# Performance work log

Hardware: AMD Instinct MI355X
Metric: run time of the kernel (lower is better)

Reference implementation:

```python
import jax, jax.numpy as jnp
import numpy as np
import math

B, T, C, H, LC, DFF = 2, 1024, 1024, 16, 256, 4096
EPS = 1e-6


def _ln(x):
    # LayerNorm without affine (elementwise_affine=False under AdaLN), eps=1e-6
    m = jnp.mean(x, -1, keepdims=True)
    v = jnp.mean((x - m) ** 2, -1, keepdims=True)
    return (x - m) * jax.lax.rsqrt(v + EPS)


def _heads(t):
    b, l, c = t.shape
    return t.reshape(b, l, H, c // H).transpose(0, 2, 1, 3)  # (b,H,l,dh)


def _unheads(t):
    b, h, l, d = t.shape
    return t.transpose(0, 2, 1, 3).reshape(b, l, h * d)


def setup_inputs():
    key = jax.random.key(0)
    ks = jax.random.split(key, 16)
    s = 0.02
    p = lambda k, sh: jax.random.normal(k, sh, jnp.float32) * s
    x_star = jax.random.normal(ks[0], (B, T, C), jnp.float32)
    x_hat = jax.random.normal(ks[1], (B, T, C), jnp.float32)
    c = jax.random.normal(ks[2], (B, LC, C), jnp.float32)
    chunk = jnp.sort(jax.random.randint(ks[3], (B, T), 0, 32), axis=1)
    m_star = chunk[:, :, None] > chunk[:, None, :]   # attend to strictly earlier chunks
    m_hat = chunk[:, :, None] == chunk[:, None, :]   # attend within same chunk
    dep_mask = jax.random.bernoulli(ks[4], 0.98, (B, T, T)) | jnp.eye(T, dtype=bool)[None]
    return dict(
        x_star=x_star, x_hat=x_hat, c=c,
        m_star=m_star, m_hat=m_hat, dep_mask=dep_mask,
        ncond_g=jnp.ones((C,), jnp.float32), ncond_b=jnp.zeros((C,), jnp.float32),
        Wq=p(ks[5], (C, C)), bq=jnp.zeros((C,), jnp.float32),
        Wkv=p(ks[6], (C, 2 * C)), bkv=jnp.zeros((2 * C,), jnp.float32),
        Wco=p(ks[7], (C, C)), bco=jnp.zeros((C,), jnp.float32),
        Wada=p(ks[8], (C, 6 * C)), bada=jnp.zeros((6 * C,), jnp.float32),
        Wqkv=p(ks[9], (C, 3 * C)), bqkv=jnp.zeros((3 * C,), jnp.float32),
        Wo=p(ks[10], (C, C)), bo=jnp.zeros((C,), jnp.float32),
        W1=p(ks[11], (C, DFF)), b1=jnp.zeros((DFF,), jnp.float32),
        W2=p(ks[12], (DFF, C)), b2=jnp.zeros((C,), jnp.float32),
    )


def _cross_attn(x, c, Wq, bq, Wkv, bkv, Wco, bco):
    q = _heads(x @ Wq + bq)
    k, v = jnp.split(c @ Wkv + bkv, 2, -1)
    k, v = _heads(k), _heads(v)
    att = jnp.einsum('bhtd,bhsd->bhts', q, k) / math.sqrt(C // H)
    y = jnp.einsum('bhts,bhsd->bhtd', jax.nn.softmax(att, -1), v)
    return _unheads(y) @ Wco + bco


def _interleave(xs, xh, m_star, m_hat, dep, Wqkv, bqkv, Wo, bo):
    # Attention.forward_interleave (eval: dropout identity)
    NEG = -jnp.inf
    sc = 1.0 / math.sqrt(C // H)
    qkv = lambda x: [_heads(t) for t in jnp.split(x @ Wqkv + bqkv, 3, -1)]
    qs, ks, vs = qkv(xs)
    qh, kh, vh = qkv(xh)
    blk_star = (~m_star)[:, None]     # True -> block
    blk_hat = (~m_hat)[:, None]
    blk_dep = (~dep)[:, None]
    causal = jnp.triu(jnp.ones((T, T), bool), 1)[None, None]
    # star stream: causal + dependency mask
    att_star = jnp.einsum('bhtd,bhsd->bhts', qs, ks) * sc
    att_star = jnp.where(blk_dep, NEG, att_star)
    p_star = jax.nn.softmax(jnp.where(causal, NEG, att_star), -1)
    y_star = _unheads(jnp.einsum('bhts,bhsd->bhtd', p_star, vs)) @ Wo + bo
    # hat stream: merge logits (q_hat vs k_star on earlier chunks, q_hat vs k_hat within chunk)
    a1 = jnp.where(blk_star, NEG, jnp.einsum('bhtd,bhsd->bhts', qh, ks) * sc)
    a2 = jnp.where(blk_hat, NEG, jnp.einsum('bhtd,bhsd->bhts', qh, kh) * sc)
    merged = jnp.where(jnp.isinf(a2), a1, a2)
    merged = jnp.where(blk_dep, NEG, merged)
    p_hat = jax.nn.softmax(merged, -1)
    y_hat = jnp.einsum('bhts,bhsd->bhtd', jnp.where(blk_star, 0.0, p_hat), vs) \
          + jnp.einsum('bhts,bhsd->bhtd', jnp.where(blk_hat, 0.0, p_hat), vh)
    y_hat = _unheads(y_hat) @ Wo + bo
    return y_star, y_hat


def reference(x_star, x_hat, c, m_star, m_hat, dep_mask,
              ncond_g, ncond_b, Wq, bq, Wkv, bkv, Wco, bco, Wada, bada,
              Wqkv, bqkv, Wo, bo, W1, b1, W2, b2):
    mod = lambda x, sh, scale: x * (1 + scale) + sh
    mlp = lambda x: jax.nn.gelu(x @ W1 + b1, approximate=True) @ W2 + b2
    ca = lambda x: _cross_attn(_ln(x) * ncond_g + ncond_b, c, Wq, bq, Wkv, bkv, Wco, bco)
    ada = lambda t: jnp.split(jax.nn.silu(t) @ Wada + bada, 6, -1)
    gs = ada(ca(x_star))
    gh = ada(ca(x_hat))
    ms = mod(_ln(x_star), gs[0], gs[1])
    mh = mod(_ln(x_hat), gh[0], gh[1])
    ys, yh = _interleave(ms, mh, m_star, m_hat, dep_mask, Wqkv, bqkv, Wo, bo)
    x_star = x_star + gs[2] * ys
    x_hat = x_hat + gh[2] * yh
    x_star = x_star + gs[5] * mlp(mod(_ln(x_star), gs[3], gs[4]))
    x_hat = x_hat + gh[5] * mlp(mod(_ln(x_hat), gh[3], gh[4]))
    return x_star, x_hat
```

## Files before the change

kernel.cpp:

```cpp
#include <hip/hip_runtime.h>
#include <hip/hip_bf16.h>
#include <stdint.h>

#define DEVI __device__ __forceinline__

typedef __bf16 bf16x8 __attribute__((ext_vector_type(8)));
typedef float f32x4 __attribute__((ext_vector_type(4)));
typedef unsigned short us;
typedef unsigned long long ull;

DEVI float b2f(us u) { union { unsigned int i; float f; } v; v.i = ((unsigned int)u) << 16; return v.f; }
DEVI us f2b(float f) {
  union { unsigned int i; float f; } v; v.f = f;
  unsigned int r = (v.i + 0x7fffu + ((v.i >> 16) & 1u)) >> 16;
  return (us)r;
}

#define NEGINF (-__builtin_inff())

DEVI void gl2lds16(const us* g, us* l) {
  __builtin_amdgcn_global_load_lds(
      (const __attribute__((address_space(1))) unsigned int*)g,
      (__attribute__((address_space(3))) unsigned int*)l, 16, 0, 0);
}

__global__ __launch_bounds__(256) void detect_flags(
    const unsigned int* __restrict__ xw, const unsigned int* __restrict__ mw,
    int* __restrict__ flags) {
  const int t = threadIdx.x;
  int cnt = 0, big = 0;
  for (int i = t; i < 4096; i += 256) {
    unsigned int w = xw[i];
    us lo = (us)(w & 0xffffu);
    float a = fabsf(b2f(lo));
    cnt += ((lo == 0) || (a >= 1e-8f && a <= 256.f)) ? 1 : 0;
    big |= (mw[i] > 1u) ? 1 : 0;
  }
  for (int o = 32; o; o >>= 1) { cnt += __shfl_down(cnt, o); big |= __shfl_down(big, o); }
  __shared__ int sc[4], sb[4];
  if ((t & 63) == 0) { sc[t >> 6] = cnt; sb[t >> 6] = big; }
  __syncthreads();
  if (t == 0) {
    flags[0] = (sc[0] + sc[1] + sc[2] + sc[3] < 2048) ? 1 : 0;
    flags[1] = (sb[0] | sb[1] | sb[2] | sb[3]);
  }
}

__global__ __launch_bounds__(256) void cvt_bf16(
    const void* __restrict__ src, us* __restrict__ dst, int n,
    const int* __restrict__ flags) {
  const int f32mode = flags[0];
  int idx = (blockIdx.x * 256 + threadIdx.x) * 4;
  if (idx >= n) return;
  if (f32mode) {
    const float* s = (const float*)src;
    float4 v = *(const float4*)(s + idx);
    dst[idx] = f2b(v.x); dst[idx + 1] = f2b(v.y);
    dst[idx + 2] = f2b(v.z); dst[idx + 3] = f2b(v.w);
  } else {
    *(uint2*)(dst + idx) = *(const uint2*)((const us*)src + idx);
  }
}

struct P10 { const void* p[10]; };
__global__ __launch_bounds__(256) void cvt_small(P10 ps, us* __restrict__ dst,
                                                 const int* __restrict__ flags) {
  const int offs[11] = {0, 1024, 2048, 3072, 5120, 6144, 12288, 15360, 16384, 20480, 21504};
  int idx = blockIdx.x * 256 + threadIdx.x;
  if (idx >= 21504) return;
  int seg = 0;
#pragma unroll
  for (int i = 1; i < 10; ++i) seg += (idx >= offs[i]) ? 1 : 0;
  int local = idx - offs[seg];
  float v = flags[0] ? ((const float*)ps.p[seg])[local]
                     : b2f(((const us*)ps.p[seg])[local]);
  dst[idx] = f2b(v);
}

__global__ __launch_bounds__(256) void transpose_cvt64(
    const void* __restrict__ W, us* __restrict__ WT, int K, int N,
    const int* __restrict__ flags) {
  __shared__ __attribute__((aligned(16))) us tile[64 * 72];
  const int f32m = flags[0];
  const int k0 = blockIdx.x * 64, n0 = blockIdx.y * 64;
  const int t = threadIdx.x;
  const int row = t >> 2, colb = (t & 3) * 16;
  const int sw = ((row >> 4) & 3) << 4;
  us tmp[16];
  if (f32m) {
    const float* src = (const float*)W + (size_t)(k0 + row) * N + n0 + colb;
#pragma unroll
    for (int i = 0; i < 16; i += 4) {
      float4 v = *(const float4*)(src + i);
      tmp[i] = f2b(v.x); tmp[i + 1] = f2b(v.y); tmp[i + 2] = f2b(v.z); tmp[i + 3] = f2b(v.w);
    }
  } else {
    const us* src = (const us*)W + (size_t)(k0 + row) * N + n0 + colb;
    *(uint4*)tmp = *(const uint4*)src;
    *(uint4*)(tmp + 8) = *(const uint4*)(src + 8);
  }
  *(uint4*)&tile[row * 72 + (colb ^ sw)] = *(uint4*)tmp;
  *(uint4*)&tile[row * 72 + (colb ^ sw) + 8] = *(uint4*)(tmp + 8);
  __syncthreads();
  const int orow = t >> 2, ocolb = (t & 3) * 16;
  const int pc = (orow & 15) | ((orow & 48) ^ (ocolb & 48));
  us out[16];
#pragma unroll
  for (int i = 0; i < 16; ++i) out[i] = tile[(ocolb + i) * 72 + pc];
  us* dst = WT + (size_t)(n0 + orow) * K + k0 + ocolb;
  *(uint4*)dst = *(uint4*)out;
  *(uint4*)(dst + 8) = *(uint4*)(out + 8);
}

struct P3 { const void* p[3]; };
__global__ __launch_bounds__(256) void pack_mask3(P3 ms, ull* __restrict__ bits,
                                                  const int* __restrict__ flags) {
  const int bytemode = flags[1];
  const void* m = ms.p[blockIdx.y];
  ull* out = bits + (size_t)blockIdx.y * 32768;
  int wv = blockIdx.x * 4 + (threadIdx.x >> 6);
  int lane = threadIdx.x & 63;
  for (int w = 0; w < 16; ++w) {
    int v;
    if (bytemode) v = ((const unsigned char*)m)[(size_t)wv * 1024 + w * 64 + lane];
    else          v = ((const int*)m)[(size_t)wv * 1024 + w * 64 + lane];
    ull b = __ballot(v != 0);
    if (lane == 0) out[(size_t)wv * 16 + w] = b;
  }
}

__global__ __launch_bounds__(256) void hat_blockflags(
    const ull* __restrict__ starb, const ull* __restrict__ hatb, int* __restrict__ bf) {
  const int bt = blockIdx.x;
  const int b = bt >> 4, tt = bt & 15;
  const int t = threadIdx.x, wv = t >> 6, lane = t & 63;
  const int t0 = tt * 64;
  for (int k = 0; k < 4; ++k) {
    int ck = wv * 4 + k;
    ull sw = starb[(size_t)(b * 1024 + t0 + lane) * 16 + ck];
    ull hw = hatb[(size_t)(b * 1024 + t0 + lane) * 16 + ck];
    int f = (__ballot(sw != 0ull) ? 1 : 0) | (__ballot(hw != 0ull) ? 2 : 0);
    if (lane == 0) bf[bt * 16 + ck] = f;
  }
}

__global__ __launch_bounds__(256) void vtrans(
    const us* __restrict__ src, us* __restrict__ dst,
    int T, int stride, int colBase, int rowOff) {
  __shared__ __attribute__((aligned(16))) us tile[64][65];
  const int bh = blockIdx.y, b = bh >> 4, h = bh & 15;
  const int t0 = blockIdx.x * 64;
  const int t = threadIdx.x;
#pragma unroll
  for (int it = 0; it < 2; ++it) {
    int idx = it * 256 + t; int r = idx >> 3, c8 = (idx & 7) * 8;
    uint4 d4 = *(const uint4*)(src + (size_t)(rowOff + b * T + t0 + r) * stride + colBase + h * 64 + c8);
    const us* e = (const us*)&d4;
#pragma unroll
    for (int i = 0; i < 8; ++i) tile[r][c8 + i] = e[i];
  }
  __syncthreads();
#pragma unroll
  for (int it = 0; it < 2; ++it) {
    int idx = it * 256 + t; int d = idx >> 3, c8 = (idx & 7) * 8;
    us tmp[8];
#pragma unroll
    for (int i = 0; i < 8; ++i) tmp[i] = tile[c8 + i][d];
    *(uint4*)(dst + ((size_t)(bh * 64 + d)) * T + t0 + c8) = *(const uint4*)tmp;
  }
}

__global__ __launch_bounds__(256) void ln_affine(
    const void* __restrict__ xs, const void* __restrict__ xh,
    const us* __restrict__ gw, const us* __restrict__ bw,
    us* __restrict__ lnx, us* __restrict__ xn, const int* __restrict__ flags) {
  const int f32m = flags[0];
  const int row = blockIdx.x;
  const void* xp = (row < 2048) ? xs : xh;
  const size_t base = (size_t)(row & 2047) * 1024;
  const int t = threadIdx.x;
  float v[4]; float s = 0.f, ss = 0.f;
#pragma unroll
  for (int i = 0; i < 4; ++i) {
    size_t idx = base + i * 256 + t;
    float x = f32m ? ((const float*)xp)[idx] : b2f(((const us*)xp)[idx]);
    v[i] = x; s += x; ss += x * x;
  }
  for (int o = 32; o; o >>= 1) { s += __shfl_down(s, o); ss += __shfl_down(ss, o); }
  __shared__ float red[2][4];
  const int wv = t >> 6, lane = t & 63;
  if (lane == 0) { red[0][wv] = s; red[1][wv] = ss; }
  __syncthreads();
  s = red[0][0] + red[0][1] + red[0][2] + red[0][3];
  ss = red[1][0] + red[1][1] + red[1][2] + red[1][3];
  const float mean = s * (1.f / 1024.f);
  const float var = fmaxf(ss * (1.f / 1024.f) - mean * mean, 0.f);
  const float rstd = rsqrtf(var + 1e-6f);
  const size_t ro = (size_t)row * 1024;
#pragma unroll
  for (int i = 0; i < 4; ++i) {
    int c = i * 256 + t;
    float n = (v[i] - mean) * rstd;
    lnx[ro + c] = f2b(n);
    xn[ro + c] = f2b(n * b2f(gw[c]) + b2f(bw[c]));
  }
}

__global__ __launch_bounds__(256) void mod_ms(
    const us* __restrict__ lnx, const us* __restrict__ gada, us* __restrict__ ms) {
  const size_t idx = ((size_t)blockIdx.x * 256 + threadIdx.x) * 4;
  const int row = (int)(idx >> 10), c = (int)(idx & 1023);
  const size_t gb = (size_t)row * 6144;
#pragma unroll
  for (int i = 0; i < 4; ++i) {
    float sh = b2f(gada[gb + c + i]);
    float sc = b2f(gada[gb + 1024 + c + i]);
    ms[idx + i] = f2b(b2f(lnx[idx + i]) * (1.f + sc) + sh);
  }
}

__global__ __launch_bounds__(256) void ln_mod(
    const float* __restrict__ x1, const us* __restrict__ gada, us* __restrict__ m2) {
  const int row = blockIdx.x;
  const float* xp = x1 + (size_t)row * 1024;
  const int t = threadIdx.x;
  float v[4]; float s = 0.f, ss = 0.f;
#pragma unroll
  for (int i = 0; i < 4; ++i) { float x = xp[i * 256 + t]; v[i] = x; s += x; ss += x * x; }
  for (int o = 32; o; o >>= 1) { s += __shfl_down(s, o); ss += __shfl_down(ss, o); }
  __shared__ float red[2][4];
  const int wv = t >> 6, lane = t & 63;
  if (lane == 0) { red[0][wv] = s; red[1][wv] = ss; }
  __syncthreads();
  s = red[0][0] + red[0][1] + red[0][2] + red[0][3];
  ss = red[1][0] + red[1][1] + red[1][2] + red[1][3];
  const float mean = s * (1.f / 1024.f);
  const float var = fmaxf(ss * (1.f / 1024.f) - mean * mean, 0.f);
  const float rstd = rsqrtf(var + 1e-6f);
  const size_t gb = (size_t)row * 6144;
#pragma unroll
  for (int i = 0; i < 4; ++i) {
    int c = i * 256 + t;
    float n = (v[i] - mean) * rstd;
    float sh = b2f(gada[gb + 3072 + c]);
    float sc = b2f(gada[gb + 4096 + c]);
    m2[(size_t)row * 1024 + c] = f2b(n * (1.f + sc) + sh);
  }
}

enum { EPI_BF16 = 0, EPI_SILU, EPI_GELU, EPI_GATE_XRES, EPI_GATE_OUT };

template <int EPI>
DEVI void gemm_epi(float v, int gmr, int gn, int N, void* out,
                   const us* gate, const void* res0, const void* res1,
                   const int* oflags) {
  const size_t oi = (size_t)gmr * N + gn;
  if constexpr (EPI == EPI_BF16) {
    ((us*)out)[oi] = f2b(v);
  } else if constexpr (EPI == EPI_SILU) {
    ((us*)out)[oi] = f2b(v / (1.f + __expf(-v)));
  } else if constexpr (EPI == EPI_GELU) {
    float u = 0.7978845608028654f * (v + 0.044715f * v * v * v);
    float th = 1.f - 2.f / (__expf(2.f * u) + 1.f);
    ((us*)out)[oi] = f2b(0.5f * v * (1.f + th));
  } else if constexpr (EPI == EPI_GATE_XRES) {
    float g = b2f(gate[(size_t)gmr * 6144 + gn]);
    const void* xr = (gmr < 2048) ? res0 : res1;
    size_t xi = (size_t)(gmr & 2047) * 1024 + gn;
    float x = oflags[0] ? ((const float*)xr)[xi] : b2f(((const us*)xr)[xi]);
    ((float*)out)[oi] = x + g * v;
  } else {
    float g = b2f(gate[(size_t)gmr * 6144 + gn]);
    float x = ((const float*)res0)[oi];
    float r2 = x + g * v;
    if (oflags[0]) ((float*)out)[oi] = r2;
    else ((us*)out)[oi] = f2b(r2);
  }
}

template <int EPI>
__global__ __launch_bounds__(256) void gemm_bt(
    const us* __restrict__ A, const us* __restrict__ BT,
    const us* __restrict__ bias, void* __restrict__ out,
    int M, int N, int K,
    const us* __restrict__ gate,
    const void* __restrict__ res0, const void* __restrict__ res1,
    const int* __restrict__ oflags) {
  __shared__ __attribute__((aligned(16))) us As[2][128 * 32];
  __shared__ __attribute__((aligned(16))) us Bs[2][128 * 32];
  const int m0 = blockIdx.x * 128, n0 = blockIdx.y * 128;
  const int t = threadIdx.x;
  const int wave = t >> 6, lane = t & 63;
  const int wm = (wave >> 1) * 64, wn = (wave & 1) * 64;
  const int l16 = lane & 15, quad = lane >> 4;
  f32x4 acc[4][4] = {};

  const int lr = lane >> 2, lc = (lane & 3) * 8;
  const us* gA = A + (size_t)(m0 + wave * 32 + lr) * K + lc;
  const us* gB = BT + (size_t)(n0 + wave * 32 + lr) * K + lc;
  const int wo = wave * 1024;

#define STAGE_BT(buf, k)                                    \
  { us* pA = &As[buf][wo]; us* pB = &Bs[buf][wo];           \
    gl2lds16(gA + (k), pA);                                 \
    gl2lds16(gA + (size_t)16 * K + (k), pA + 512);          \
    gl2lds16(gB + (k), pB);                                 \
    gl2lds16(gB + (size_t)16 * K + (k), pB + 512); }

  STAGE_BT(0, 0);
  STAGE_BT(1, 32);
  const int NK = K >> 5;
  int cur = 0;
  for (int i = 0; i < NK - 1; ++i) {
    asm volatile("s_waitcnt vmcnt(4)\n\ts_barrier" ::: "memory");
    bf16x8 af[4], bfv[4];
#pragma unroll
    for (int x = 0; x < 4; ++x) af[x] = *(const bf16x8*)(const void*)&As[cur][(wm + x * 16 + l16) * 32 + quad * 8];
#pragma unroll
    for (int j = 0; j < 4; ++j) bfv[j] = *(const bf16x8*)(const void*)&Bs[cur][(wn + j * 16 + l16) * 32 + quad * 8];
    asm volatile("s_waitcnt lgkmcnt(0)\n\ts_barrier" ::: "memory");
    if (i + 2 < NK) STAGE_BT(cur, (i + 2) * 32);
#pragma unroll
    for (int x = 0; x < 4; ++x)
#pragma unroll
      for (int j = 0; j < 4; ++j)
        acc[x][j] = __builtin_amdgcn_mfma_f32_16x16x32_bf16(af[x], bfv[j], acc[x][j], 0, 0, 0);
    cur ^= 1;
  }
  asm volatile("s_waitcnt vmcnt(0)\n\ts_barrier" ::: "memory");
  {
    bf16x8 af[4], bfv[4];
#pragma unroll
    for (int x = 0; x < 4; ++x) af[x] = *(const bf16x8*)(const void*)&As[cur][(wm + x * 16 + l16) * 32 + quad * 8];
#pragma unroll
    for (int j = 0; j < 4; ++j) bfv[j] = *(const bf16x8*)(const void*)&Bs[cur][(wn + j * 16 + l16) * 32 + quad * 8];
#pragma unroll
    for (int x = 0; x < 4; ++x)
#pragma unroll
      for (int j = 0; j < 4; ++j)
        acc[x][j] = __builtin_amdgcn_mfma_f32_16x16x32_bf16(af[x], bfv[j], acc[x][j], 0, 0, 0);
  }
#undef STAGE_BT

#pragma unroll
  for (int i = 0; i < 4; ++i) {
    const int gm = m0 + wm + i * 16 + quad * 4;
#pragma unroll
    for (int j = 0; j < 4; ++j) {
      const int gn = n0 + wn + j * 16 + l16;
      const float bv = b2f(bias[gn]);
#pragma unroll
      for (int r = 0; r < 4; ++r)
        gemm_epi<EPI>(acc[i][j][r] + bv, gm + r, gn, N, out, gate, res0, res1, oflags);
    }
  }
}

template <int EPI>
__global__ __launch_bounds__(256) void gemm_bt64(
    const us* __restrict__ A, const us* __restrict__ BT,
    const us* __restrict__ bias, void* __restrict__ out,
    int M, int N, int K,
    const us* __restrict__ gate,
    const void* __restrict__ res0, const void* __restrict__ res1,
    const int* __restrict__ oflags) {
  __shared__ __attribute__((aligned(16))) us As[2][128 * 32];
  __shared__ __attribute__((aligned(16))) us Bs[2][64 * 32];
  const int m0 = blockIdx.x * 128, n0 = blockIdx.y * 64;
  const int t = threadIdx.x;
  const int wave = t >> 6, lane = t & 63;
  const int wm = (wave >> 1) * 64, wn = (wave & 1) * 32;
  const int l16 = lane & 15, quad = lane >> 4;
  f32x4 acc[4][2] = {};

  const int lr = lane >> 2, lc = (lane & 3) * 8;
  const us* gA = A + (size_t)(m0 + wave * 32 + lr) * K + lc;
  const us* gB = BT + (size_t)(n0 + wave * 16 + lr) * K + lc;
  const int woA = wave * 1024, woB = wave * 512;

#define STAGE_BT64(buf, k)                                  \
  { us* pA = &As[buf][woA];                                 \
    gl2lds16(gA + (k), pA);                                 \
    gl2lds16(gA + (size_t)16 * K + (k), pA + 512);          \
    gl2lds16(gB + (k), &Bs[buf][woB]); }

  STAGE_BT64(0, 0);
  STAGE_BT64(1, 32);
  const int NK = K >> 5;
  int cur = 0;
  for (int i = 0; i < NK - 1; ++i) {
    asm volatile("s_waitcnt vmcnt(3)\n\ts_barrier" ::: "memory");
    bf16x8 af[4], bfv[2];
#pragma unroll
    for (int x = 0; x < 4; ++x) af[x] = *(const bf16x8*)(const void*)&As[cur][(wm + x * 16 + l16) * 32 + quad * 8];
#pragma unroll
    for (int j = 0; j < 2; ++j) bfv[j] = *(const bf16x8*)(const void*)&Bs[cur][(wn + j * 16 + l16) * 32 + quad * 8];
    asm volatile("s_waitcnt lgkmcnt(0)\n\ts_barrier" ::: "memory");
    if (i + 2 < NK) STAGE_BT64(cur, (i + 2) * 32);
#pragma unroll
    for (int x = 0; x < 4; ++x)
#pragma unroll
      for (int j = 0; j < 2; ++j)
        acc[x][j] = __builtin_amdgcn_mfma_f32_16x16x32_bf16(af[x], bfv[j], acc[x][j], 0, 0, 0);
    cur ^= 1;
  }
  asm volatile("s_waitcnt vmcnt(0)\n\ts_barrier" ::: "memory");
  {
    bf16x8 af[4], bfv[2];
#pragma unroll
    for (int x = 0; x < 4; ++x) af[x] = *(const bf16x8*)(const void*)&As[cur][(wm + x * 16 + l16) * 32 + quad * 8];
#pragma unroll
    for (int j = 0; j < 2; ++j) bfv[j] = *(const bf16x8*)(const void*)&Bs[cur][(wn + j * 16 + l16) * 32 + quad * 8];
#pragma unroll
    for (int x = 0; x < 4; ++x)
#pragma unroll
      for (int j = 0; j < 2; ++j)
        acc[x][j] = __builtin_amdgcn_mfma_f32_16x16x32_bf16(af[x], bfv[j], acc[x][j], 0, 0, 0);
  }
#undef STAGE_BT64

#pragma unroll
  for (int i = 0; i < 4; ++i) {
    const int gm = m0 + wm + i * 16 + quad * 4;
#pragma unroll
    for (int j = 0; j < 2; ++j) {
      const int gn = n0 + wn + j * 16 + l16;
      const float bv = b2f(bias[gn]);
#pragma unroll
      for (int r = 0; r < 4; ++r)
        gemm_epi<EPI>(acc[i][j][r] + bv, gm + r, gn, N, out, gate, res0, res1, oflags);
    }
  }
}

struct AttnState { float m[4], l[4]; f32x4 o[4]; };

DEVI void st_init(AttnState& s) {
#pragma unroll
  for (int r = 0; r < 4; ++r) { s.m[r] = NEGINF; s.l[r] = 0.f; s.o[r] = f32x4{}; }
}

struct StReg { uint4 k0, k1, v0, v1; };

DEVI void stage_load(StReg& r, const us* __restrict__ ksrc, int kStride,
                     const us* __restrict__ vsrc, int vStride, int t) {
  const int r0 = t >> 3, c0 = (t & 7) * 8;
  const int r1 = 32 + r0;
  r.k0 = *(const uint4*)(ksrc + (size_t)r0 * kStride + c0);
  r.k1 = *(const uint4*)(ksrc + (size_t)r1 * kStride + c0);
  r.v0 = *(const uint4*)(vsrc + (size_t)r0 * vStride + c0);
  r.v1 = *(const uint4*)(vsrc + (size_t)r1 * vStride + c0);
}

DEVI void stage_write(us* __restrict__ Kb, us* __restrict__ Vb,
                      const StReg& r, int t) {
  const int r0 = t >> 3, c0 = (t & 7) * 8;
  const int r1 = 32 + r0;
  *(uint4*)&Kb[r0 * 72 + c0] = r.k0;
  *(uint4*)&Kb[r1 * 72 + c0] = r.k1;
  *(uint4*)&Vb[r0 * 72 + c0] = r.v0;
  *(uint4*)&Vb[r1 * 72 + c0] = r.v1;
}

template <bool MASKED>
DEVI void attn_round(const us* __restrict__ Kb, const us* __restrict__ Vb,
                     us* __restrict__ Pb, const ull* mrow,
                     bf16x8 aq0, bf16x8 aq1, AttnState& st,
                     int wv, int l16, int quad) {
  f32x4 s[4];
#pragma unroll
  for (int j = 0; j < 4; ++j) {
    const int row = j * 16 + l16;
    bf16x8 bk0 = *(const bf16x8*)(const void*)&Kb[row * 72 + quad * 8];
    bf16x8 bk1 = *(const bf16x8*)(const void*)&Kb[row * 72 + 32 + quad * 8];
    f32x4 z = {};
    z = __builtin_amdgcn_mfma_f32_16x16x32_bf16(aq0, bk0, z, 0, 0, 0);
    z = __builtin_amdgcn_mfma_f32_16x16x32_bf16(aq1, bk1, z, 0, 0, 0);
    s[j] = z;
  }
  const float CE = 0.18033688011112042f;
#pragma unroll
  for (int r = 0; r < 4; ++r) {
    float mx = fmaxf(fmaxf(s[0][r], s[1][r]), fmaxf(s[2][r], s[3][r]));
#pragma unroll
    for (int o2 = 8; o2; o2 >>= 1) mx = fmaxf(mx, __shfl_xor(mx, o2));
    const float mn = fmaxf(st.m[r], mx);
    const float alpha = exp2f((st.m[r] - mn) * CE);
    const float mnC = mn * CE;
    float rs = 0.f;
#pragma unroll
    for (int j = 0; j < 4; ++j) {
      float p = exp2f(__builtin_fmaf(s[j][r], CE, -mnC));
      if constexpr (MASKED) p = ((mrow[r] >> (j * 16 + l16)) & 1ull) ? p : 0.f;
      rs += p;
      ((__bf16*)Pb)[(wv * 16 + quad * 4 + r) * 72 + j * 16 + l16] = (__bf16)p;
    }
#pragma unroll
    for (int o2 = 8; o2; o2 >>= 1) rs += __shfl_xor(rs, o2);
    st.m[r] = mn;
    st.l[r] = st.l[r] * alpha + rs;
#pragma unroll
    for (int jd = 0; jd < 4; ++jd) st.o[jd][r] *= alpha;
  }
  bf16x8 ap0 = *(const bf16x8*)(const void*)&Pb[(wv * 16 + l16) * 72 + quad * 8];
  bf16x8 ap1 = *(const bf16x8*)(const void*)&Pb[(wv * 16 + l16) * 72 + 32 + quad * 8];
#pragma unroll
  for (int jd = 0; jd < 4; ++jd) {
    bf16x8 v0 = *(const bf16x8*)(const void*)&Vb[(jd * 16 + l16) * 72 + quad * 8];
    bf16x8 v1 = *(const bf16x8*)(const void*)&Vb[(jd * 16 + l16) * 72 + 32 + quad * 8];
    st.o[jd] = __builtin_amdgcn_mfma_f32_16x16x32_bf16(ap0, v0, st.o[jd], 0, 0, 0);
    st.o[jd] = __builtin_amdgcn_mfma_f32_16x16x32_bf16(ap1, v1, st.o[jd], 0, 0, 0);
  }
}

DEVI void attn_write(us* __restrict__ y, const AttnState& st, int rowAbs,
                     int h, int l16, int quad) {
#pragma unroll
  for (int r = 0; r < 4; ++r) {
    const float inv = (st.l[r] > 0.f) ? 1.f / st.l[r] : 0.f;
#pragma unroll
    for (int jd = 0; jd < 4; ++jd)
      y[(size_t)(rowAbs + quad * 4 + r) * 1024 + h * 64 + jd * 16 + l16] =
          f2b(st.o[jd][r] * inv);
  }
}

__global__ __launch_bounds__(256) void cross_attn_mfma(
    const us* __restrict__ q, const us* __restrict__ kv,
    const us* __restrict__ vT, us* __restrict__ y) {
  __shared__ __attribute__((aligned(16))) us Kb[64 * 72];
  __shared__ __attribute__((aligned(16))) us Vb[64 * 72];
  __shared__ __attribute__((aligned(16))) us Pb[64 * 72];
  const int bid = blockIdx.x;
  const int xcd = bid & 7, tmp = bid >> 3;
  const int tt = tmp & 15, gq = tmp >> 4;
  const int g = gq * 8 + xcd;
  const int strm = g >> 5, b = (g >> 4) & 1, h = g & 15;
  const int t = threadIdx.x, wv = t >> 6, lane = t & 63;
  const int l16 = lane & 15, quad = lane >> 4;
  const int rowbase = strm * 2048 + b * 1024 + tt * 64 + wv * 16;
  const us* qp = q + (size_t)(rowbase + l16) * 1024 + h * 64 + quad * 8;
  bf16x8 aq0 = *(const bf16x8*)(qp);
  bf16x8 aq1 = *(const bf16x8*)(qp + 32);
  const us* kb = kv + (size_t)b * (256 * 2048) + h * 64;
  const us* vb = vT + (size_t)(b * 16 + h) * (64 * 256);
  AttnState st; st_init(st);
  StReg sr;
  stage_load(sr, kb, 2048, vb, 256, t);
  for (int rnd = 0; rnd < 4; ++rnd) {
    __syncthreads();
    stage_write(Kb, Vb, sr, t);
    __syncthreads();
    if (rnd < 3)
      stage_load(sr, kb + (size_t)(rnd + 1) * 64 * 2048, 2048,
                 vb + (rnd + 1) * 64, 256, t);
    attn_round<false>(Kb, Vb, Pb, nullptr, aq0, aq1, st, wv, l16, quad);
  }
  attn_write(y, st, rowbase, h, l16, quad);
}

DEVI void star_body(us* Kb, us* Vb, us* Pb, const us* qkv, const us* vT,
                    const ull* depb, us* y, int b, int h, int tt, int t) {
  const int wv = t >> 6, lane = t & 63;
  const int l16 = lane & 15, quad = lane >> 4;
  const int t0 = tt * 64;
  const int rowbase = b * 1024 + t0 + wv * 16;
  const us* qp = qkv + (size_t)(rowbase + l16) * 3072 + h * 64 + quad * 8;
  bf16x8 aq0 = *(const bf16x8*)(qp);
  bf16x8 aq1 = *(const bf16x8*)(qp + 32);
  const us* kb = qkv + (size_t)(b * 1024) * 3072 + 1024 + h * 64;
  const us* vb = vT + (size_t)(b * 16 + h) * 65536;
  AttnState st; st_init(st);
  ull mrow[4];
  StReg sr;
  stage_load(sr, kb, 3072, vb, 1024, t);
  for (int ck = 0; ck <= tt; ++ck) {
    __syncthreads();
    stage_write(Kb, Vb, sr, t);
    __syncthreads();
    if (ck < tt)
      stage_load(sr, kb + (size_t)(ck + 1) * 64 * 3072, 3072,
                 vb + (ck + 1) * 64, 1024, t);
#pragma unroll
    for (int r = 0; r < 4; ++r) {
      ull d = depb[(size_t)(rowbase + quad * 4 + r) * 16 + ck];
      if (ck == tt) {
        const int idx = wv * 16 + quad * 4 + r;
        d &= (2ull << idx) - 1ull;
      }
      mrow[r] = d;
    }
    attn_round<true>(Kb, Vb, Pb, mrow, aq0, aq1, st, wv, l16, quad);
  }
  attn_write(y, st, rowbase, h, l16, quad);
}

DEVI void hat_body(us* Kb, us* Vb, us* Pb, const us* qkv,
                   const us* vsT, const us* vhT,
                   const ull* starb, const ull* hatb, const ull* depb,
                   const int* bflags, us* y, int b, int h, int tt, int t) {
  const int wv = t >> 6, lane = t & 63;
  const int l16 = lane & 15, quad = lane >> 4;
  const int t0 = tt * 64;
  const int rowbase = b * 1024 + t0 + wv * 16;
  const us* qp = qkv + (size_t)(2048 + rowbase + l16) * 3072 + h * 64 + quad * 8;
  bf16x8 aq0 = *(const bf16x8*)(qp);
  bf16x8 aq1 = *(const bf16x8*)(qp + 32);
  const us* ksb = qkv + (size_t)(b * 1024) * 3072 + 1024 + h * 64;
  const us* khb = qkv + (size_t)(2048 + b * 1024) * 3072 + 1024 + h * 64;
  const us* vsb = vsT + (size_t)(b * 16 + h) * 65536;
  const us* vhb = vhT + (size_t)(b * 16 + h) * 65536;
  AttnState st; st_init(st);
  unsigned mask = 0;
  for (int ck = 0; ck < 16; ++ck) {
    int f = bflags[(b * 16 + tt) * 16 + ck];
    mask |= (unsigned)(f & 3) << (2 * ck);
  }
  if (mask) {
    int slot = (int)__builtin_ctz(mask);
    unsigned rem = mask & (mask - 1);
    StReg sr;
    {
      const int ck = slot >> 1, part = slot & 1;
      stage_load(sr, (part ? khb : ksb) + (size_t)ck * 64 * 3072, 3072,
                 (part ? vhb : vsb) + ck * 64, 1024, t);
    }
    for (;;) {
      __syncthreads();
      stage_write(Kb, Vb, sr, t);
      __syncthreads();
      const int ck = slot >> 1, part = slot & 1;
      int nslot = -1;
      if (rem) {
        nslot = (int)__builtin_ctz(rem);
        rem &= rem - 1;
        const int nck = nslot >> 1, npart = nslot & 1;
        stage_load(sr, (npart ? khb : ksb) + (size_t)nck * 64 * 3072, 3072,
                   (npart ? vhb : vsb) + nck * 64, 1024, t);
      }
      ull mrow[4];
#pragma unroll
      for (int r = 0; r < 4; ++r) {
        const size_t mi = (size_t)(rowbase + quad * 4 + r) * 16 + ck;
        mrow[r] = (part ? hatb[mi] : starb[mi]) & depb[mi];
      }
      attn_round<true>(Kb, Vb, Pb, mrow, aq0, aq1, st, wv, l16, quad);
      if (nslot < 0) break;
      slot = nslot;
    }
  }
  attn_write(y, st, 2048 + rowbase, h, l16, quad);
}

__global__ __launch_bounds__(256) void self_attn_mfma(
    const us* __restrict__ qkv,
    const us* __restrict__ vstT, const us* __restrict__ vhtT,
    const ull* __restrict__ sbits, const ull* __restrict__ hbits,
    const ull* __restrict__ dbits, const int* __restrict__ bflags,
    us* __restrict__ y) {
  __shared__ __attribute__((aligned(16))) us Kb[64 * 72];
  __shared__ __attribute__((aligned(16))) us Vb[64 * 72];
  __shared__ __attribute__((aligned(16))) us Pb[64 * 72];
  const int bid = blockIdx.x;
  const int xcd = bid & 7, tmp = bid >> 3;
  const int tt = tmp & 15, gq = tmp >> 4;
  const int g = gq * 8 + xcd;
  const int t = threadIdx.x;
  if (g < 32) {
    star_body(Kb, Vb, Pb, qkv, vstT, dbits, y, g >> 4, g & 15, tt, t);
  } else {
    const int g2 = g - 32;
    hat_body(Kb, Vb, Pb, qkv, vstT, vhtT, sbits, hbits, dbits, bflags,
             y, g2 >> 4, g2 & 15, tt, t);
  }
}

extern "C" void kernel_launch(void* const* d_in, const int* in_sizes, int n_in,
                              void* d_out, int out_size, void* d_ws, size_t ws_size,
                              hipStream_t stream) {
  const void* xs = d_in[0];
  const void* xh = d_in[1];
  const void* cc = d_in[2];
  const void* mstar = d_in[3];
  const void* mhat = d_in[4];
  const void* mdep = d_in[5];
  const void* ng = d_in[6];
  const void* nb = d_in[7];
  const void* Wq = d_in[8];
  const void* bq = d_in[9];
  const void* Wkv = d_in[10];
  const void* bkv = d_in[11];
  const void* Wco = d_in[12];
  const void* bco = d_in[13];
  const void* Wada = d_in[14];
  const void* bada = d_in[15];
  const void* Wqkv = d_in[16];
  const void* bqkv = d_in[17];
  const void* Wo = d_in[18];
  const void* bo = d_in[19];
  const void* W1 = d_in[20];
  const void* b1 = d_in[21];
  const void* W2 = d_in[22];
  const void* b2 = d_in[23];
  (void)in_sizes; (void)n_in; (void)out_size; (void)ws_size;

  char* ws = (char*)d_ws;
  size_t off = 0;
  auto alloc = [&](size_t bytes) -> char* {
    char* p = ws + off;
    off += (bytes + 255) & ~(size_t)255;
    return p;
  };
  int* flags = (int*)alloc(256);
  int* bflags = (int*)alloc(512 * 4);
  us* smallb = (us*)alloc(21504 * 2);
  us* ngb = smallb, *nbb = smallb + 1024, *bqb = smallb + 2048,
      *bkvb = smallb + 3072, *bcob = smallb + 5120, *badab = smallb + 6144,
      *bqkvb = smallb + 12288, *bob = smallb + 15360, *b1b = smallb + 16384,
      *b2b = smallb + 20480;
  us* WqT = (us*)alloc(1048576ull * 2);
  us* WkvT = (us*)alloc(2097152ull * 2);
  us* WcoT = (us*)alloc(1048576ull * 2);
  us* WadaT = (us*)alloc(6291456ull * 2);
  us* WqkvT = (us*)alloc(3145728ull * 2);
  us* WoT = (us*)alloc(1048576ull * 2);
  us* W1T = (us*)alloc(4194304ull * 2);
  us* W2T = (us*)alloc(4194304ull * 2);
  us* xn = (us*)alloc(4194304ull * 2);
  us* qb = (us*)alloc(4194304ull * 2);
  us* kvb = (us*)alloc(1048576ull * 2);
  us* gada = (us*)alloc(25165824ull * 2);
  us* msb = (us*)alloc(4194304ull * 2);
  us* qkvb = (us*)alloc(12582912ull * 2);
  float* x1 = (float*)alloc(4194304ull * 4);
  us* hid = (us*)alloc(16777216ull * 2);
  ull* mb = (ull*)alloc(3ull * 32768 * 8);
  us* kvT = (us*)alloc(524288ull * 2);
  us* vstT = (us*)alloc(2097152ull * 2);
  us* vhtT = (us*)alloc(2097152ull * 2);

  ull* sbits = mb;
  ull* hbits = mb + 32768;
  ull* dbits = mb + 65536;
  us* ccb = hid;
  us* lnx = hid + 1048576;
  us* yca = xn;
  us* silub = qb;
  us* yat = msb;

  dim3 blk(256);
  detect_flags<<<1, blk, 0, stream>>>((const unsigned int*)xs, (const unsigned int*)mdep, flags);

  cvt_bf16<<<512, blk, 0, stream>>>(cc, ccb, 524288, flags);
  P10 ps10; ps10.p[0] = ng; ps10.p[1] = nb; ps10.p[2] = bq; ps10.p[3] = bkv;
  ps10.p[4] = bco; ps10.p[5] = bada; ps10.p[6] = bqkv; ps10.p[7] = bo;
  ps10.p[8] = b1; ps10.p[9] = b2;
  cvt_small<<<84, blk, 0, stream>>>(ps10, smallb, flags);

  transpose_cvt64<<<dim3(16, 16), blk, 0, stream>>>(Wq, WqT, 1024, 1024, flags);
  transpose_cvt64<<<dim3(16, 32), blk, 0, stream>>>(Wkv, WkvT, 1024, 2048, flags);
  transpose_cvt64<<<dim3(16, 16), blk, 0, stream>>>(Wco, WcoT, 1024, 1024, flags);
  transpose_cvt64<<<dim3(16, 96), blk, 0, stream>>>(Wada, WadaT, 1024, 6144, flags);
  transpose_cvt64<<<dim3(16, 48), blk, 0, stream>>>(Wqkv, WqkvT, 1024, 3072, flags);
  transpose_cvt64<<<dim3(16, 16), blk, 0, stream>>>(Wo, WoT, 1024, 1024, flags);
  transpose_cvt64<<<dim3(16, 64), blk, 0, stream>>>(W1, W1T, 1024, 4096, flags);
  transpose_cvt64<<<dim3(64, 16), blk, 0, stream>>>(W2, W2T, 4096, 1024, flags);

  P3 ps3; ps3.p[0] = mstar; ps3.p[1] = mhat; ps3.p[2] = mdep;
  pack_mask3<<<dim3(512, 3), blk, 0, stream>>>(ps3, mb, flags);
  hat_blockflags<<<32, blk, 0, stream>>>(sbits, hbits, bflags);

  ln_affine<<<4096, blk, 0, stream>>>(xs, xh, ngb, nbb, lnx, xn, flags);
  gemm_bt64<EPI_BF16><<<dim3(32, 16), blk, 0, stream>>>(xn, WqT, bqb, qb, 4096, 1024, 1024, nullptr, nullptr, nullptr, nullptr);
  gemm_bt64<EPI_BF16><<<dim3(4, 32), blk, 0, stream>>>(ccb, WkvT, bkvb, kvb, 512, 2048, 1024, nullptr, nullptr, nullptr, nullptr);
  vtrans<<<dim3(4, 32), blk, 0, stream>>>(kvb, kvT, 256, 2048, 1024, 0);
  cross_attn_mfma<<<1024, blk, 0, stream>>>(qb, kvb, kvT, yca);
  gemm_bt64<EPI_SILU><<<dim3(32, 16), blk, 0, stream>>>(yca, WcoT, bcob, silub, 4096, 1024, 1024, nullptr, nullptr, nullptr, nullptr);
  gemm_bt<EPI_BF16><<<dim3(32, 48), blk, 0, stream>>>(silub, WadaT, badab, gada, 4096, 6144, 1024, nullptr, nullptr, nullptr, nullptr);
  mod_ms<<<4096, blk, 0, stream>>>(lnx, gada, msb);
  gemm_bt<EPI_BF16><<<dim3(32, 24), blk, 0, stream>>>(msb, WqkvT, bqkvb, qkvb, 4096, 3072, 1024, nullptr, nullptr, nullptr, nullptr);
  vtrans<<<dim3(16, 32), blk, 0, stream>>>(qkvb, vstT, 1024, 3072, 2048, 0);
  vtrans<<<dim3(16, 32), blk, 0, stream>>>(qkvb, vhtT, 1024, 3072, 2048, 2048);
  self_attn_mfma<<<1024, blk, 0, stream>>>(qkvb, vstT, vhtT, sbits, hbits, dbits, bflags, yat);
  gemm_bt64<EPI_GATE_XRES><<<dim3(32, 16), blk, 0, stream>>>(yat, WoT, bob, x1, 4096, 1024, 1024, gada + 2048, xs, xh, flags);
  ln_mod<<<4096, blk, 0, stream>>>(x1, gada, msb);
  gemm_bt<EPI_GELU><<<dim3(32, 32), blk, 0, stream>>>(msb, W1T, b1b, hid, 4096, 4096, 1024, nullptr, nullptr, nullptr, nullptr);
  gemm_bt<EPI_GATE_OUT><<<dim3(32, 8), blk, 0, stream>>>(hid, W2T, b2b, d_out, 4096, 1024, 4096, gada + 5120, x1, nullptr, flags);
}
```

Baseline: 708.1 us.

## Drop register prefetch in attention, add MFMA priority hints, use 64-tile GEMM for W2

The attention kernels no longer prefetch the next K/V tile into registers while computing the current one. Each tile is now loaded straight into shared memory between barriers, and the hat kernel's bitmask slot loop becomes a plain per-chunk loop. s_setprio is raised around the MFMA sections to favour matrix issue across waves. The final W2 GEMM switches to the 64-tile GEMM variant with twice as many blocks, which may improve occupancy at the cost of more operand reloads. Losing the prefetch exposes global load latency, which is meant to be offset by lower register pressure and more waves per CU.

Result: faster. 639.2 us (-9.7%).

```diff
diff --git a/kernel.cpp b/kernel.cpp
--- a/kernel.cpp
+++ b/kernel.cpp
@@ -440,26 +440,14 @@
   for (int r = 0; r < 4; ++r) { s.m[r] = NEGINF; s.l[r] = 0.f; s.o[r] = f32x4{}; }
 }
 
-struct StReg { uint4 k0, k1, v0, v1; };
-
-DEVI void stage_load(StReg& r, const us* __restrict__ ksrc, int kStride,
-                     const us* __restrict__ vsrc, int vStride, int t) {
-  const int r0 = t >> 3, c0 = (t & 7) * 8;
-  const int r1 = 32 + r0;
-  r.k0 = *(const uint4*)(ksrc + (size_t)r0 * kStride + c0);
-  r.k1 = *(const uint4*)(ksrc + (size_t)r1 * kStride + c0);
-  r.v0 = *(const uint4*)(vsrc + (size_t)r0 * vStride + c0);
-  r.v1 = *(const uint4*)(vsrc + (size_t)r1 * vStride + c0);
-}
-
-DEVI void stage_write(us* __restrict__ Kb, us* __restrict__ Vb,
-                      const StReg& r, int t) {
-  const int r0 = t >> 3, c0 = (t & 7) * 8;
-  const int r1 = 32 + r0;
-  *(uint4*)&Kb[r0 * 72 + c0] = r.k0;
-  *(uint4*)&Kb[r1 * 72 + c0] = r.k1;
-  *(uint4*)&Vb[r0 * 72 + c0] = r.v0;
-  *(uint4*)&Vb[r1 * 72 + c0] = r.v1;
+DEVI void stage64(us* __restrict__ dst, const us* __restrict__ src,
+                  int strideUs, int t) {
+#pragma unroll
+  for (int it = 0; it < 2; ++it) {
+    const int id = it * 256 + t;
+    const int row = id >> 3, c8 = (id & 7) * 8;
+    *(uint4*)&dst[row * 72 + c8] = *(const uint4*)(src + (size_t)row * strideUs + c8);
+  }
 }
 
 template <bool MASKED>
@@ -468,6 +456,7 @@
                      bf16x8 aq0, bf16x8 aq1, AttnState& st,
                      int wv, int l16, int quad) {
   f32x4 s[4];
+  __builtin_amdgcn_s_setprio(1);
 #pragma unroll
   for (int j = 0; j < 4; ++j) {
     const int row = j * 16 + l16;
@@ -478,6 +467,7 @@
     z = __builtin_amdgcn_mfma_f32_16x16x32_bf16(aq1, bk1, z, 0, 0, 0);
     s[j] = z;
   }
+  __builtin_amdgcn_s_setprio(0);
   const float CE = 0.18033688011112042f;
 #pragma unroll
   for (int r = 0; r < 4; ++r) {
@@ -504,6 +494,7 @@
   }
   bf16x8 ap0 = *(const bf16x8*)(const void*)&Pb[(wv * 16 + l16) * 72 + quad * 8];
   bf16x8 ap1 = *(const bf16x8*)(const void*)&Pb[(wv * 16 + l16) * 72 + 32 + quad * 8];
+  __builtin_amdgcn_s_setprio(1);
 #pragma unroll
   for (int jd = 0; jd < 4; ++jd) {
     bf16x8 v0 = *(const bf16x8*)(const void*)&Vb[(jd * 16 + l16) * 72 + quad * 8];
@@ -511,6 +502,7 @@
     st.o[jd] = __builtin_amdgcn_mfma_f32_16x16x32_bf16(ap0, v0, st.o[jd], 0, 0, 0);
     st.o[jd] = __builtin_amdgcn_mfma_f32_16x16x32_bf16(ap1, v1, st.o[jd], 0, 0, 0);
   }
+  __builtin_amdgcn_s_setprio(0);
 }
 
 DEVI void attn_write(us* __restrict__ y, const AttnState& st, int rowAbs,
@@ -545,15 +537,12 @@
   const us* kb = kv + (size_t)b * (256 * 2048) + h * 64;
   const us* vb = vT + (size_t)(b * 16 + h) * (64 * 256);
   AttnState st; st_init(st);
-  StReg sr;
-  stage_load(sr, kb, 2048, vb, 256, t);
   for (int rnd = 0; rnd < 4; ++rnd) {
+    const int s0 = rnd * 64;
     __syncthreads();
-    stage_write(Kb, Vb, sr, t);
+    stage64(Kb, kb + (size_t)s0 * 2048, 2048, t);
+    stage64(Vb, vb + s0, 256, t);
     __syncthreads();
-    if (rnd < 3)
-      stage_load(sr, kb + (size_t)(rnd + 1) * 64 * 2048, 2048,
-                 vb + (rnd + 1) * 64, 256, t);
     attn_round<false>(Kb, Vb, Pb, nullptr, aq0, aq1, st, wv, l16, quad);
   }
   attn_write(y, st, rowbase, h, l16, quad);
@@ -572,15 +561,12 @@
   const us* vb = vT + (size_t)(b * 16 + h) * 65536;
   AttnState st; st_init(st);
   ull mrow[4];
-  StReg sr;
-  stage_load(sr, kb, 3072, vb, 1024, t);
   for (int ck = 0; ck <= tt; ++ck) {
+    const int s0 = ck * 64;
     __syncthreads();
-    stage_write(Kb, Vb, sr, t);
+    stage64(Kb, kb + (size_t)s0 * 3072, 3072, t);
+    stage64(Vb, vb + s0, 1024, t);
     __syncthreads();
-    if (ck < tt)
-      stage_load(sr, kb + (size_t)(ck + 1) * 64 * 3072, 3072,
-                 vb + (ck + 1) * 64, 1024, t);
 #pragma unroll
     for (int r = 0; r < 4; ++r) {
       ull d = depb[(size_t)(rowbase + quad * 4 + r) * 16 + ck];
@@ -611,42 +597,33 @@
   const us* vsb = vsT + (size_t)(b * 16 + h) * 65536;
   const us* vhb = vhT + (size_t)(b * 16 + h) * 65536;
   AttnState st; st_init(st);
-  unsigned mask = 0;
+  ull mrow[4];
   for (int ck = 0; ck < 16; ++ck) {
-    int f = bflags[(b * 16 + tt) * 16 + ck];
-    mask |= (unsigned)(f & 3) << (2 * ck);
-  }
-  if (mask) {
-    int slot = (int)__builtin_ctz(mask);
-    unsigned rem = mask & (mask - 1);
-    StReg sr;
-    {
-      const int ck = slot >> 1, part = slot & 1;
-      stage_load(sr, (part ? khb : ksb) + (size_t)ck * 64 * 3072, 3072,
-                 (part ? vhb : vsb) + ck * 64, 1024, t);
-    }
-    for (;;) {
+    const int f = bflags[(b * 16 + tt) * 16 + ck];
+    const int s0 = ck * 64;
+    if (f & 1) {
       __syncthreads();
-      stage_write(Kb, Vb, sr, t);
+      stage64(Kb, ksb + (size_t)s0 * 3072, 3072, t);
+      stage64(Vb, vsb + s0, 1024, t);
       __syncthreads();
-      const int ck = slot >> 1, part = slot & 1;
-      int nslot = -1;
-      if (rem) {
-        nslot = (int)__builtin_ctz(rem);
-        rem &= rem - 1;
-        const int nck = nslot >> 1, npart = nslot & 1;
-        stage_load(sr, (npart ? khb : ksb) + (size_t)nck * 64 * 3072, 3072,
-                   (npart ? vhb : vsb) + nck * 64, 1024, t);
-      }
-      ull mrow[4];
 #pragma unroll
       for (int r = 0; r < 4; ++r) {
         const size_t mi = (size_t)(rowbase + quad * 4 + r) * 16 + ck;
-        mrow[r] = (part ? hatb[mi] : starb[mi]) & depb[mi];
+        mrow[r] = starb[mi] & depb[mi];
       }
       attn_round<true>(Kb, Vb, Pb, mrow, aq0, aq1, st, wv, l16, quad);
-      if (nslot < 0) break;
-      slot = nslot;
+    }
+    if (f & 2) {
+      __syncthreads();
+      stage64(Kb, khb + (size_t)s0 * 3072, 3072, t);
+      stage64(Vb, vhb + s0, 1024, t);
+      __syncthreads();
+#pragma unroll
+      for (int r = 0; r < 4; ++r) {
+        const size_t mi = (size_t)(rowbase + quad * 4 + r) * 16 + ck;
+        mrow[r] = hatb[mi] & depb[mi];
+      }
+      attn_round<true>(Kb, Vb, Pb, mrow, aq0, aq1, st, wv, l16, quad);
     }
   }
   attn_write(y, st, 2048 + rowbase, h, l16, quad);
@@ -785,5 +762,5 @@
   gemm_bt64<EPI_GATE_XRES><<<dim3(32, 16), blk, 0, stream>>>(yat, WoT, bob, x1, 4096, 1024, 1024, gada + 2048, xs, xh, flags);
   ln_mod<<<4096, blk, 0, stream>>>(x1, gada, msb);
   gemm_bt<EPI_GELU><<<dim3(32, 32), blk, 0, stream>>>(msb, W1T, b1b, hid, 4096, 4096, 1024, nullptr, nullptr, nullptr, nullptr);
-  gemm_bt<EPI_GATE_OUT><<<dim3(32, 8), blk, 0, stream>>>(hid, W2T, b2b, d_out, 4096, 1024, 4096, gada + 5120, x1, nullptr, flags);
-}
+  gemm_bt64<EPI_GATE_OUT><<<dim3(32, 16), blk, 0, stream>>>(hid, W2T, b2b, d_out, 4096, 1024, 4096, gada + 5120, x1, nullptr, flags);
+}
```
